# Optimization experiments

Measured on AMD Instinct MI355X. Metric: run time of the kernel, lower is better.

The kernel has to match this reference:

```python
import jax, jax.numpy as jnp
import numpy as np

N_HEAD = 16
D_MODEL = 1024


def setup_inputs() -> dict:
    key = jax.random.key(0)
    ks = jax.random.split(key, 12)
    B, S, D = 2, 2048, D_MODEL
    s = 0.02
    return {
        "q": jax.random.normal(ks[0], (B, S, D), jnp.float32),
        "k": jax.random.normal(ks[1], (B, S, D), jnp.float32),
        "v": jax.random.normal(ks[2], (B, S, 2 * D), jnp.float32),
        "Wq": jax.random.normal(ks[3], (D, D), jnp.float32) * s,
        "bq": jnp.zeros((D,), jnp.float32),
        "Wk": jax.random.normal(ks[4], (D, D), jnp.float32) * s,
        "bk": jnp.zeros((D,), jnp.float32),
        "Wv": jax.random.normal(ks[5], (2 * D, D), jnp.float32) * s,
        "bv": jnp.zeros((D,), jnp.float32),
        "Wfc": jax.random.normal(ks[6], (D, 2 * D), jnp.float32) * s,
        "bfc": jnp.zeros((2 * D,), jnp.float32),
        "padding_mask": jnp.ones((B, S), jnp.int32),
    }


def reference(q, k, v, Wq, bq, Wk, bk, Wv, bv, Wfc, bfc, padding_mask):
    B, S, D = q.shape
    H = N_HEAD
    dh = D // H
    scale = jnp.float32(np.sqrt(dh))
    # projections, split heads -> [B, H, S, dh]
    qh = (q @ Wq + bq).reshape(B, S, H, dh).transpose(0, 2, 1, 3)
    kh = (k @ Wk + bk).reshape(B, S, H, dh).transpose(0, 2, 1, 3)
    vh = (v @ Wv + bv).reshape(B, S, H, dh).transpose(0, 2, 1, 3)
    # scores [B, H, S, S]
    attn = jnp.einsum("bhqd,bhkd->bhqk", qh, kh) / scale
    pad = (padding_mask == 0)[:, None, None, :]  # [B,1,1,S]
    attn = jnp.where(pad, -jnp.inf, attn)
    attn = jax.nn.softmax(attn, axis=-1)
    # dropout p=0 in eval -> identity
    out = jnp.einsum("bhqk,bhkd->bhqd", attn, vh)
    out = out.transpose(0, 2, 1, 3).reshape(B, S, D)
    out = out @ Wfc + bfc  # [B, S, 2D]
    attn_avg = attn.sum(axis=1) / H  # [B, S, S]
    return out, attn_avg
```

## Files before the change

kernel.cpp:

```cpp
#include <hip/hip_runtime.h>
#include <math.h>

#define BATCH   2
#define SLEN    2048
#define DMODEL  1024
#define NHEAD   16
#define DHEAD   64
#define DOUT    2048
#define MROWS   (BATCH * SLEN)
#define NSPLIT  2
#define KSPAN   (SLEN / NSPLIT)

typedef short bf16x8 __attribute__((ext_vector_type(8)));
typedef float floatx4 __attribute__((ext_vector_type(4)));

static __device__ __forceinline__ unsigned short f2bf(float f) {
  unsigned u = __float_as_uint(f);
  u += 0x7fff + ((u >> 16) & 1);
  return (unsigned short)(u >> 16);
}
static __device__ __forceinline__ float bf2f(unsigned short s) {
  return __uint_as_float(((unsigned)s) << 16);
}
static __device__ __forceinline__ floatx4 mfma16(bf16x8 a, bf16x8 b, floatx4 c) {
  return __builtin_amdgcn_mfma_f32_16x16x32_bf16(a, b, c, 0, 0, 0);
}
static __device__ __forceinline__ void gll16(const void* g, void* l) {
  __builtin_amdgcn_global_load_lds(
      (const __attribute__((address_space(1))) unsigned int*)g,
      (__attribute__((address_space(3))) unsigned int*)l, 16, 0, 0);
}

__global__ __launch_bounds__(256) void conv_bf16_k(
    const float* __restrict__ in, unsigned short* __restrict__ out, int n8) {
  const int i = blockIdx.x * 256 + threadIdx.x;
  if (i >= n8) return;
  const float4 a = ((const float4*)in)[i * 2];
  const float4 b = ((const float4*)in)[i * 2 + 1];
  ushort4 u0, u1;
  u0.x = f2bf(a.x); u0.y = f2bf(a.y); u0.z = f2bf(a.z); u0.w = f2bf(a.w);
  u1.x = f2bf(b.x); u1.y = f2bf(b.y); u1.z = f2bf(b.z); u1.w = f2bf(b.w);
  ((ushort4*)out)[i * 2] = u0;
  ((ushort4*)out)[i * 2 + 1] = u1;
}

__global__ __launch_bounds__(256) void wtrans_k(
    const float* __restrict__ W, unsigned short* __restrict__ WT, int K, int N) {
  __shared__ float T[32][33];
  const int t = threadIdx.x;
  const int n0 = blockIdx.x * 32, k0 = blockIdx.y * 32;
  {
    const int r = t >> 3, c4 = (t & 7) * 4;
    const float4 w = *(const float4*)(W + (size_t)(k0 + r) * N + n0 + c4);
    T[r][c4 + 0] = w.x; T[r][c4 + 1] = w.y; T[r][c4 + 2] = w.z; T[r][c4 + 3] = w.w;
  }
  __syncthreads();
  {
    const int n = t >> 3, k4 = (t & 7) * 4;
    ushort4 u;
    u.x = f2bf(T[k4 + 0][n]); u.y = f2bf(T[k4 + 1][n]);
    u.z = f2bf(T[k4 + 2][n]); u.w = f2bf(T[k4 + 3][n]);
    *(ushort4*)(WT + (size_t)(n0 + n) * K + k0 + k4) = u;
  }
}

template <int MODE>
static __device__ __forceinline__ void gemm_body(
    const unsigned short* __restrict__ A, const unsigned short* __restrict__ BT,
    const float* __restrict__ bias, void* __restrict__ C, int M, int K, int N,
    int row0, int col0) {
  __shared__ unsigned short As[128 * 64];
  __shared__ unsigned short Bs[64 * 64];
  const int t = threadIdx.x;
  const int w = t >> 6, l = t & 63, quad = l >> 4, lq = l & 15;
  const int wm = (w >> 1) * 64, wn = (w & 1) * 32;

  const unsigned short* aS[4];
#pragma unroll
  for (int jj = 0; jj < 4; jj++) {
    const int inst = w * 4 + jj;
    const int m = inst * 8 + (l >> 3);
    const int g = l & 7;
    aS[jj] = A + (size_t)(row0 + m) * K + ((g ^ (m & 7)) << 3);
  }
  const unsigned short* bS[2];
#pragma unroll
  for (int jj = 0; jj < 2; jj++) {
    const int inst = w * 2 + jj;
    const int n = inst * 8 + (l >> 3);
    const int g = l & 7;
    bS[jj] = BT + (size_t)(col0 + n) * K + ((g ^ (n & 7)) << 3);
  }

  floatx4 acc[4][2];
#pragma unroll
  for (int i = 0; i < 4; i++)
#pragma unroll
    for (int j = 0; j < 2; j++) acc[i][j] = (floatx4){0.f, 0.f, 0.f, 0.f};

  for (int kt = 0; kt < K; kt += 64) {
#pragma unroll
    for (int jj = 0; jj < 4; jj++)
      gll16(aS[jj] + kt, As + (w * 4 + jj) * 512);
#pragma unroll
    for (int jj = 0; jj < 2; jj++)
      gll16(bS[jj] + kt, Bs + (w * 2 + jj) * 512);
    __syncthreads();

    bf16x8 af[4][2], bfr[2][2];
#pragma unroll
    for (int ti = 0; ti < 4; ti++) {
      const int m = wm + ti * 16 + lq;
#pragma unroll
      for (int h = 0; h < 2; h++)
        af[ti][h] = *(const bf16x8*)(As + m * 64 + (((h * 4 + quad) ^ (m & 7)) << 3));
    }
#pragma unroll
    for (int tj = 0; tj < 2; tj++) {
      const int n = wn + tj * 16 + lq;
#pragma unroll
      for (int h = 0; h < 2; h++)
        bfr[tj][h] = *(const bf16x8*)(Bs + n * 64 + (((h * 4 + quad) ^ (n & 7)) << 3));
    }
#pragma unroll
    for (int ti = 0; ti < 4; ti++)
#pragma unroll
      for (int tj = 0; tj < 2; tj++) {
        acc[ti][tj] = mfma16(af[ti][0], bfr[tj][0], acc[ti][tj]);
        acc[ti][tj] = mfma16(af[ti][1], bfr[tj][1], acc[ti][tj]);
      }
    __syncthreads();
  }

#pragma unroll
  for (int tj = 0; tj < 2; tj++) {
    const int col = col0 + wn + tj * 16 + lq;
    const float bv = bias[col];
    if (MODE == 2) {
#pragma unroll
      for (int ti = 0; ti < 4; ti++) {
        ushort4 u;
        u.x = f2bf(acc[ti][tj][0] + bv);
        u.y = f2bf(acc[ti][tj][1] + bv);
        u.z = f2bf(acc[ti][tj][2] + bv);
        u.w = f2bf(acc[ti][tj][3] + bv);
        *(ushort4*)((unsigned short*)C + (size_t)col * M + row0 + wm + ti * 16 +
                    quad * 4) = u;
      }
    } else {
#pragma unroll
      for (int ti = 0; ti < 4; ti++)
#pragma unroll
        for (int r = 0; r < 4; r++) {
          const int row = row0 + wm + ti * 16 + quad * 4 + r;
          const float vv = acc[ti][tj][r] + bv;
          if (MODE == 1)
            ((float*)C)[(size_t)row * N + col] = vv;
          else
            ((unsigned short*)C)[(size_t)row * N + col] = f2bf(vv);
        }
    }
  }
}

__global__ __launch_bounds__(256) void qkproj_k(
    const unsigned short* qb, const unsigned short* kb,
    const unsigned short* WqT, const unsigned short* WkT,
    const float* bq, const float* bk,
    unsigned short* Qp, unsigned short* Kp) {
  const int z = blockIdx.z;
  gemm_body<0>(z ? kb : qb, z ? WkT : WqT, z ? bk : bq, z ? Kp : Qp,
               MROWS, DMODEL, DMODEL, blockIdx.y * 128, blockIdx.x * 64);
}
__global__ __launch_bounds__(256) void vproj_k(
    const unsigned short* vb, const unsigned short* WvT, const float* bv,
    unsigned short* VT) {
  gemm_body<2>(vb, WvT, bv, VT, MROWS, 2 * DMODEL, DMODEL,
               blockIdx.y * 128, blockIdx.x * 64);
}
__global__ __launch_bounds__(256) void fc_k(
    const unsigned short* att, const unsigned short* WfcT, const float* bfc,
    float* out) {
  gemm_body<1>(att, WfcT, bfc, out, MROWS, DMODEL, DOUT,
               blockIdx.y * 128, blockIdx.x * 64);
}

__global__ __launch_bounds__(256) void flash_mfma_k(
    const unsigned short* __restrict__ Qp, const unsigned short* __restrict__ Kp,
    const unsigned short* __restrict__ VT, const int* __restrict__ mask,
    unsigned short* __restrict__ Opart, float* __restrict__ Lpart) {
  __shared__ unsigned short Ks[64 * 88];
  __shared__ unsigned short Vs[64 * 88];
  __shared__ unsigned short Ps[4 * 16 * 64];
  const int t = threadIdx.x;
  const int w = t >> 6, l = t & 63, quad = l >> 4, lq = l & 15;
  const int q0 = blockIdx.x * 64;
  const int h = blockIdx.y >> 1, split = blockIdx.y & 1;
  const int b = blockIdx.z;

  const unsigned short* qptr =
      Qp + (size_t)(b * SLEN + q0 + w * 16 + lq) * DMODEL + h * 64;
  const bf16x8 aq0 = *(const bf16x8*)(qptr + quad * 8);
  const bf16x8 aq1 = *(const bf16x8*)(qptr + 32 + quad * 8);

  floatx4 acc_o[4];
#pragma unroll
  for (int dj = 0; dj < 4; dj++) acc_o[dj] = (floatx4){0.f, 0.f, 0.f, 0.f};
  float lsum[4] = {0.f, 0.f, 0.f, 0.f};

  const int krow = t >> 2, kseg = (t & 3) * 16;

  for (int k0 = split * KSPAN; k0 < split * KSPAN + KSPAN; k0 += 64) {
    __syncthreads();
    const unsigned short* kg =
        Kp + (size_t)(b * SLEN + k0 + krow) * DMODEL + h * 64 + kseg;
    *(bf16x8*)&Ks[krow * 88 + kseg]     = *(const bf16x8*)kg;
    *(bf16x8*)&Ks[krow * 88 + kseg + 8] = *(const bf16x8*)(kg + 8);
#pragma unroll
    for (int p = 0; p < 2; p++) {
      const int d = (p * 256 + t) >> 3, s8 = (t & 7) * 8;
      *(bf16x8*)&Vs[d * 88 + s8] =
          *(const bf16x8*)(VT + (size_t)(h * 64 + d) * MROWS + b * SLEN + k0 + s8);
    }
    __syncthreads();

    floatx4 s[4];
    int mk[4];
#pragma unroll
    for (int ti = 0; ti < 4; ti++) {
      const bf16x8 bk0 = *(const bf16x8*)&Ks[(ti * 16 + lq) * 88 + quad * 8];
      const bf16x8 bk1 = *(const bf16x8*)&Ks[(ti * 16 + lq) * 88 + 32 + quad * 8];
      floatx4 z = (floatx4){0.f, 0.f, 0.f, 0.f};
      z = mfma16(aq0, bk0, z);
      z = mfma16(aq1, bk1, z);
      s[ti] = z;
      mk[ti] = mask[b * SLEN + k0 + ti * 16 + lq];
    }
#pragma unroll
    for (int ti = 0; ti < 4; ti++)
#pragma unroll
      for (int r = 0; r < 4; r++) {
        float e = __expf(s[ti][r] * 0.125f);
        e = mk[ti] ? e : 0.f;
        s[ti][r] = e;
        lsum[r] += e;
      }
#pragma unroll
    for (int ti = 0; ti < 4; ti++)
#pragma unroll
      for (int r = 0; r < 4; r++) {
        const int qq = quad * 4 + r;
        Ps[w * 1024 + qq * 64 + ((ti * 16 + lq + qq * 8) & 63)] = f2bf(s[ti][r]);
      }
    const bf16x8 ap0 =
        *(const bf16x8*)&Ps[w * 1024 + lq * 64 + 8 * ((quad + lq) & 7)];
    const bf16x8 ap1 =
        *(const bf16x8*)&Ps[w * 1024 + lq * 64 + 8 * ((quad + lq + 4) & 7)];
#pragma unroll
    for (int dj = 0; dj < 4; dj++) {
      const bf16x8 bv0 = *(const bf16x8*)&Vs[(dj * 16 + lq) * 88 + quad * 8];
      const bf16x8 bv1 = *(const bf16x8*)&Vs[(dj * 16 + lq) * 88 + 32 + quad * 8];
      acc_o[dj] = mfma16(ap0, bv0, acc_o[dj]);
      acc_o[dj] = mfma16(ap1, bv1, acc_o[dj]);
    }
  }

#pragma unroll
  for (int r = 0; r < 4; r++) {
    float v = lsum[r];
    v += __shfl_xor(v, 1);
    v += __shfl_xor(v, 2);
    v += __shfl_xor(v, 4);
    v += __shfl_xor(v, 8);
    lsum[r] = v;
  }

  const size_t obase =
      (((size_t)split * BATCH + b) * NHEAD + h) * SLEN + q0 + w * 16;
#pragma unroll
  for (int dj = 0; dj < 4; dj++)
#pragma unroll
    for (int r = 0; r < 4; r++)
      Opart[(obase + quad * 4 + r) * DHEAD + dj * 16 + lq] = f2bf(acc_o[dj][r]);
  if (lq == 0) {
#pragma unroll
    for (int r = 0; r < 4; r++)
      Lpart[obase + quad * 4 + r] = lsum[r];
  }
}

__global__ __launch_bounds__(256) void combine_k(
    const unsigned short* __restrict__ Opart, const float* __restrict__ Lpart,
    unsigned short* __restrict__ att, float* __restrict__ lbuf) {
  const int gid = blockIdx.x * 256 + threadIdx.x;
  const int row = gid >> 3;
  const int d8 = (gid & 7) * 8;
  const float l0 = Lpart[row];
  const float l1 = Lpart[(size_t)BATCH * NHEAD * SLEN + row];
  const float lt = l0 + l1;
  const float il = (lt > 0.f) ? 1.f / lt : 0.f;
  const bf16x8 o0 = *(const bf16x8*)(Opart + (size_t)row * DHEAD + d8);
  const bf16x8 o1 = *(const bf16x8*)(Opart + (size_t)(BATCH * NHEAD * SLEN) * DHEAD +
                                     (size_t)row * DHEAD + d8);
  const int b = row >> 15, hh = (row >> 11) & 15, q = row & 2047;
  unsigned short* dst = att + (size_t)(b * SLEN + q) * DMODEL + hh * 64 + d8;
  ushort4 u0, u1;
  float vv[8];
#pragma unroll
  for (int j = 0; j < 8; j++)
    vv[j] = (bf2f((unsigned short)o0[j]) + bf2f((unsigned short)o1[j])) * il;
  u0.x = f2bf(vv[0]); u0.y = f2bf(vv[1]); u0.z = f2bf(vv[2]); u0.w = f2bf(vv[3]);
  u1.x = f2bf(vv[4]); u1.y = f2bf(vv[5]); u1.z = f2bf(vv[6]); u1.w = f2bf(vv[7]);
  ((ushort4*)dst)[0] = u0;
  ((ushort4*)dst)[1] = u1;
  if ((gid & 7) == 0) lbuf[row] = lt;
}

__global__ __launch_bounds__(256) void attn_avg_mfma_k(
    const unsigned short* __restrict__ Qp, const unsigned short* __restrict__ Kp,
    const float* __restrict__ lbuf, const int* __restrict__ mask,
    float* __restrict__ aout) {
  __shared__ unsigned short Ks[64 * 88];
  const int t = threadIdx.x;
  const int w = t >> 6, l = t & 63, quad = l >> 4, lq = l & 15;
  const int k0 = blockIdx.x * 64, q0 = blockIdx.y * 64, b = blockIdx.z;

  floatx4 acc[4];
#pragma unroll
  for (int ti = 0; ti < 4; ti++) acc[ti] = (floatx4){0.f, 0.f, 0.f, 0.f};
  int mk[4];
#pragma unroll
  for (int ti = 0; ti < 4; ti++) mk[ti] = mask[b * SLEN + k0 + ti * 16 + lq];

  const unsigned short* qbase =
      Qp + (size_t)(b * SLEN + q0 + w * 16 + lq) * DMODEL;
  const int krow = t >> 2, kseg = (t & 3) * 16;

  for (int h = 0; h < NHEAD; h++) {
    __syncthreads();
    const unsigned short* kg =
        Kp + (size_t)(b * SLEN + k0 + krow) * DMODEL + h * 64 + kseg;
    *(bf16x8*)&Ks[krow * 88 + kseg]     = *(const bf16x8*)kg;
    *(bf16x8*)&Ks[krow * 88 + kseg + 8] = *(const bf16x8*)(kg + 8);
    __syncthreads();

    const bf16x8 aq0 = *(const bf16x8*)(qbase + h * 64 + quad * 8);
    const bf16x8 aq1 = *(const bf16x8*)(qbase + h * 64 + 32 + quad * 8);
    float ilr[4];
#pragma unroll
    for (int r = 0; r < 4; r++) {
      const float lv = lbuf[(b * NHEAD + h) * SLEN + q0 + w * 16 + quad * 4 + r];
      ilr[r] = (lv > 0.f) ? 1.f / lv : 0.f;
    }
#pragma unroll
    for (int ti = 0; ti < 4; ti++) {
      const bf16x8 bk0 = *(const bf16x8*)&Ks[(ti * 16 + lq) * 88 + quad * 8];
      const bf16x8 bk1 = *(const bf16x8*)&Ks[(ti * 16 + lq) * 88 + 32 + quad * 8];
      floatx4 z = (floatx4){0.f, 0.f, 0.f, 0.f};
      z = mfma16(aq0, bk0, z);
      z = mfma16(aq1, bk1, z);
#pragma unroll
      for (int r = 0; r < 4; r++)
        acc[ti][r] += mk[ti] ? __expf(z[r] * 0.125f) * ilr[r] : 0.f;
    }
  }
  const float ih = 1.f / NHEAD;
#pragma unroll
  for (int ti = 0; ti < 4; ti++)
#pragma unroll
    for (int r = 0; r < 4; r++)
      aout[(size_t)(b * SLEN + q0 + w * 16 + quad * 4 + r) * SLEN + k0 +
           ti * 16 + lq] = acc[ti][r] * ih;
}

extern "C" void kernel_launch(void* const* d_in, const int* in_sizes, int n_in,
                              void* d_out, int out_size, void* d_ws, size_t ws_size,
                              hipStream_t stream) {
  const float* q   = (const float*)d_in[0];
  const float* k   = (const float*)d_in[1];
  const float* v   = (const float*)d_in[2];
  const float* Wq  = (const float*)d_in[3];
  const float* bq  = (const float*)d_in[4];
  const float* Wk  = (const float*)d_in[5];
  const float* bk  = (const float*)d_in[6];
  const float* Wv  = (const float*)d_in[7];
  const float* bv  = (const float*)d_in[8];
  const float* Wfc = (const float*)d_in[9];
  const float* bfc = (const float*)d_in[10];
  const int* mask  = (const int*)d_in[11];

  float* out      = (float*)d_out;
  float* attn_avg = out + (size_t)MROWS * DOUT;

  unsigned short* qb = (unsigned short*)d_out;
  unsigned short* kb = qb + (1u << 22);
  unsigned short* vb = kb + (1u << 22);
  unsigned short* Opart = (unsigned short*)d_out;
  float* Lpart = (float*)((char*)d_out + (size_t)NSPLIT * BATCH * NHEAD * SLEN * DHEAD * 2);

  unsigned short* wsb  = (unsigned short*)d_ws;
  unsigned short* WqT  = wsb;
  unsigned short* WkT  = wsb + (1u << 20);
  unsigned short* WvT  = wsb + (2u << 20);
  unsigned short* WfcT = wsb + (4u << 20);
  unsigned short* Qp   = wsb + (6u << 20);
  unsigned short* Kp   = Qp + (1u << 22);
  unsigned short* VT   = Kp + (1u << 22);
  unsigned short* att  = VT + (1u << 22);
  float* lbuf = (float*)(att + (1u << 22));

  conv_bf16_k<<<dim3(2048), dim3(256), 0, stream>>>(q, qb, (1 << 22) / 8);
  conv_bf16_k<<<dim3(2048), dim3(256), 0, stream>>>(k, kb, (1 << 22) / 8);
  conv_bf16_k<<<dim3(4096), dim3(256), 0, stream>>>(v, vb, (1 << 23) / 8);
  wtrans_k<<<dim3(32, 32), dim3(256), 0, stream>>>(Wq, WqT, DMODEL, DMODEL);
  wtrans_k<<<dim3(32, 32), dim3(256), 0, stream>>>(Wk, WkT, DMODEL, DMODEL);
  wtrans_k<<<dim3(32, 64), dim3(256), 0, stream>>>(Wv, WvT, 2 * DMODEL, DMODEL);
  wtrans_k<<<dim3(64, 32), dim3(256), 0, stream>>>(Wfc, WfcT, DMODEL, DOUT);
  qkproj_k<<<dim3(DMODEL / 64, MROWS / 128, 2), dim3(256), 0, stream>>>(
      qb, kb, WqT, WkT, bq, bk, Qp, Kp);
  vproj_k<<<dim3(DMODEL / 64, MROWS / 128), dim3(256), 0, stream>>>(
      vb, WvT, bv, VT);
  flash_mfma_k<<<dim3(SLEN / 64, NHEAD * NSPLIT, BATCH), dim3(256), 0, stream>>>(
      Qp, Kp, VT, mask, Opart, Lpart);
  combine_k<<<dim3(BATCH * NHEAD * SLEN * DHEAD / 8 / 256), dim3(256), 0, stream>>>(
      Opart, Lpart, att, lbuf);
  attn_avg_mfma_k<<<dim3(SLEN / 64, SLEN / 64, BATCH), dim3(256), 0, stream>>>(
      Qp, Kp, lbuf, mask, attn_avg);
  fc_k<<<dim3(DOUT / 64, MROWS / 128), dim3(256), 0, stream>>>(
      att, WfcT, bfc, out);
}
```

Baseline: 397.6 us.

## Merge conversion launches and use async swizzled LDS loads in attention kernels

```diff
diff --git a/kernel.cpp b/kernel.cpp
--- a/kernel.cpp
+++ b/kernel.cpp
@@ -31,24 +31,42 @@
       (__attribute__((address_space(3))) unsigned int*)l, 16, 0, 0);
 }
 
-__global__ __launch_bounds__(256) void conv_bf16_k(
-    const float* __restrict__ in, unsigned short* __restrict__ out, int n8) {
-  const int i = blockIdx.x * 256 + threadIdx.x;
-  if (i >= n8) return;
-  const float4 a = ((const float4*)in)[i * 2];
-  const float4 b = ((const float4*)in)[i * 2 + 1];
+__global__ __launch_bounds__(256) void conv_all_k(
+    const float* __restrict__ q, const float* __restrict__ k,
+    const float* __restrict__ v, unsigned short* __restrict__ qb,
+    unsigned short* __restrict__ kb, unsigned short* __restrict__ vb) {
+  int i = blockIdx.x * 256 + threadIdx.x;
+  const float* src;
+  unsigned short* dst;
+  if (i < (1 << 19)) { src = q; dst = qb; }
+  else if (i < (1 << 20)) { src = k; dst = kb; i -= 1 << 19; }
+  else { src = v; dst = vb; i -= 1 << 20; }
+  const float4 a = ((const float4*)src)[i * 2];
+  const float4 b = ((const float4*)src)[i * 2 + 1];
   ushort4 u0, u1;
   u0.x = f2bf(a.x); u0.y = f2bf(a.y); u0.z = f2bf(a.z); u0.w = f2bf(a.w);
   u1.x = f2bf(b.x); u1.y = f2bf(b.y); u1.z = f2bf(b.z); u1.w = f2bf(b.w);
-  ((ushort4*)out)[i * 2] = u0;
-  ((ushort4*)out)[i * 2 + 1] = u1;
-}
-
-__global__ __launch_bounds__(256) void wtrans_k(
-    const float* __restrict__ W, unsigned short* __restrict__ WT, int K, int N) {
+  ((ushort4*)dst)[i * 2] = u0;
+  ((ushort4*)dst)[i * 2 + 1] = u1;
+}
+
+__global__ __launch_bounds__(256) void wtrans_all_k(
+    const float* __restrict__ Wq, const float* __restrict__ Wk,
+    const float* __restrict__ Wv, const float* __restrict__ Wfc,
+    unsigned short* __restrict__ WqT, unsigned short* __restrict__ WkT,
+    unsigned short* __restrict__ WvT, unsigned short* __restrict__ WfcT) {
   __shared__ float T[32][33];
+  int id = blockIdx.x;
+  const float* W;
+  unsigned short* WT;
+  int K, N;
+  if (id < 1024)      { W = Wq;  WT = WqT;  K = 1024; N = 1024; }
+  else if (id < 2048) { W = Wk;  WT = WkT;  K = 1024; N = 1024; id -= 1024; }
+  else if (id < 4096) { W = Wv;  WT = WvT;  K = 2048; N = 1024; id -= 2048; }
+  else                { W = Wfc; WT = WfcT; K = 1024; N = 2048; id -= 4096; }
+  const int ntn = N / 32;
+  const int n0 = (id % ntn) * 32, k0 = (id / ntn) * 32;
   const int t = threadIdx.x;
-  const int n0 = blockIdx.x * 32, k0 = blockIdx.y * 32;
   {
     const int r = t >> 3, c4 = (t & 7) * 4;
     const float4 w = *(const float4*)(W + (size_t)(k0 + r) * N + n0 + c4);
@@ -78,18 +96,14 @@
   const unsigned short* aS[4];
 #pragma unroll
   for (int jj = 0; jj < 4; jj++) {
-    const int inst = w * 4 + jj;
-    const int m = inst * 8 + (l >> 3);
-    const int g = l & 7;
-    aS[jj] = A + (size_t)(row0 + m) * K + ((g ^ (m & 7)) << 3);
+    const int m = (w * 4 + jj) * 8 + (l >> 3);
+    aS[jj] = A + (size_t)(row0 + m) * K + (((l & 7) ^ (m & 7)) << 3);
   }
   const unsigned short* bS[2];
 #pragma unroll
   for (int jj = 0; jj < 2; jj++) {
-    const int inst = w * 2 + jj;
-    const int n = inst * 8 + (l >> 3);
-    const int g = l & 7;
-    bS[jj] = BT + (size_t)(col0 + n) * K + ((g ^ (n & 7)) << 3);
+    const int n = (w * 2 + jj) * 8 + (l >> 3);
+    bS[jj] = BT + (size_t)(col0 + n) * K + (((l & 7) ^ (n & 7)) << 3);
   }
 
   floatx4 acc[4][2];
@@ -189,9 +203,9 @@
     const unsigned short* __restrict__ Qp, const unsigned short* __restrict__ Kp,
     const unsigned short* __restrict__ VT, const int* __restrict__ mask,
     unsigned short* __restrict__ Opart, float* __restrict__ Lpart) {
-  __shared__ unsigned short Ks[64 * 88];
-  __shared__ unsigned short Vs[64 * 88];
-  __shared__ unsigned short Ps[4 * 16 * 64];
+  __shared__ unsigned short Ks[64 * 64];
+  __shared__ unsigned short Vs[64 * 64];
+  __shared__ unsigned short Ps[4][16 * 68];
   const int t = threadIdx.x;
   const int w = t >> 6, l = t & 63, quad = l >> 4, lq = l & 15;
   const int q0 = blockIdx.x * 64;
@@ -203,77 +217,72 @@
   const bf16x8 aq0 = *(const bf16x8*)(qptr + quad * 8);
   const bf16x8 aq1 = *(const bf16x8*)(qptr + 32 + quad * 8);
 
+  int krow[2], kchunk[2];
+#pragma unroll
+  for (int jj = 0; jj < 2; jj++) {
+    krow[jj] = (w * 2 + jj) * 8 + (l >> 3);
+    kchunk[jj] = (l & 7) ^ (krow[jj] & 7);
+  }
+  const unsigned short* Kbase = Kp + (size_t)b * SLEN * DMODEL + h * 64;
+  const unsigned short* Vbase = VT + (size_t)h * 64 * MROWS + b * SLEN;
+
   floatx4 acc_o[4];
 #pragma unroll
   for (int dj = 0; dj < 4; dj++) acc_o[dj] = (floatx4){0.f, 0.f, 0.f, 0.f};
-  float lsum[4] = {0.f, 0.f, 0.f, 0.f};
-
-  const int krow = t >> 2, kseg = (t & 3) * 16;
+  float lsum = 0.f;
+  unsigned short* PsW = &Ps[w][0];
 
   for (int k0 = split * KSPAN; k0 < split * KSPAN + KSPAN; k0 += 64) {
     __syncthreads();
-    const unsigned short* kg =
-        Kp + (size_t)(b * SLEN + k0 + krow) * DMODEL + h * 64 + kseg;
-    *(bf16x8*)&Ks[krow * 88 + kseg]     = *(const bf16x8*)kg;
-    *(bf16x8*)&Ks[krow * 88 + kseg + 8] = *(const bf16x8*)(kg + 8);
-#pragma unroll
-    for (int p = 0; p < 2; p++) {
-      const int d = (p * 256 + t) >> 3, s8 = (t & 7) * 8;
-      *(bf16x8*)&Vs[d * 88 + s8] =
-          *(const bf16x8*)(VT + (size_t)(h * 64 + d) * MROWS + b * SLEN + k0 + s8);
-    }
-    __syncthreads();
-
-    floatx4 s[4];
-    int mk[4];
+#pragma unroll
+    for (int jj = 0; jj < 2; jj++) {
+      const int inst = w * 2 + jj;
+      gll16(Kbase + (size_t)(k0 + krow[jj]) * DMODEL + kchunk[jj] * 8,
+            Ks + inst * 512);
+      gll16(Vbase + (size_t)krow[jj] * MROWS + k0 + kchunk[jj] * 8,
+            Vs + inst * 512);
+    }
+    __syncthreads();
+
 #pragma unroll
     for (int ti = 0; ti < 4; ti++) {
-      const bf16x8 bk0 = *(const bf16x8*)&Ks[(ti * 16 + lq) * 88 + quad * 8];
-      const bf16x8 bk1 = *(const bf16x8*)&Ks[(ti * 16 + lq) * 88 + 32 + quad * 8];
+      const int kk = ti * 16 + lq;
+      const bf16x8 bk0 = *(const bf16x8*)(Ks + kk * 64 + ((quad ^ (kk & 7)) << 3));
+      const bf16x8 bk1 =
+          *(const bf16x8*)(Ks + kk * 64 + (((4 + quad) ^ (kk & 7)) << 3));
       floatx4 z = (floatx4){0.f, 0.f, 0.f, 0.f};
-      z = mfma16(aq0, bk0, z);
-      z = mfma16(aq1, bk1, z);
-      s[ti] = z;
-      mk[ti] = mask[b * SLEN + k0 + ti * 16 + lq];
-    }
-#pragma unroll
-    for (int ti = 0; ti < 4; ti++)
+      z = mfma16(bk0, aq0, z);
+      z = mfma16(bk1, aq1, z);
+      const int4 m4 = *(const int4*)(mask + b * SLEN + k0 + ti * 16 + quad * 4);
+      const int mv[4] = {m4.x, m4.y, m4.z, m4.w};
+      float e[4];
 #pragma unroll
       for (int r = 0; r < 4; r++) {
-        float e = __expf(s[ti][r] * 0.125f);
-        e = mk[ti] ? e : 0.f;
-        s[ti][r] = e;
-        lsum[r] += e;
+        float ev = __expf(z[r] * 0.125f);
+        ev = mv[r] ? ev : 0.f;
+        e[r] = ev;
+        lsum += ev;
       }
-#pragma unroll
-    for (int ti = 0; ti < 4; ti++)
-#pragma unroll
-      for (int r = 0; r < 4; r++) {
-        const int qq = quad * 4 + r;
-        Ps[w * 1024 + qq * 64 + ((ti * 16 + lq + qq * 8) & 63)] = f2bf(s[ti][r]);
-      }
-    const bf16x8 ap0 =
-        *(const bf16x8*)&Ps[w * 1024 + lq * 64 + 8 * ((quad + lq) & 7)];
-    const bf16x8 ap1 =
-        *(const bf16x8*)&Ps[w * 1024 + lq * 64 + 8 * ((quad + lq + 4) & 7)];
+      ushort4 u;
+      u.x = f2bf(e[0]); u.y = f2bf(e[1]); u.z = f2bf(e[2]); u.w = f2bf(e[3]);
+      *(ushort4*)(PsW + lq * 68 + ti * 16 + quad * 4) = u;
+    }
+    __asm__ __volatile__("" ::: "memory");
+    const bf16x8 ap0 = *(const bf16x8*)(PsW + lq * 68 + quad * 8);
+    const bf16x8 ap1 = *(const bf16x8*)(PsW + lq * 68 + 32 + quad * 8);
 #pragma unroll
     for (int dj = 0; dj < 4; dj++) {
-      const bf16x8 bv0 = *(const bf16x8*)&Vs[(dj * 16 + lq) * 88 + quad * 8];
-      const bf16x8 bv1 = *(const bf16x8*)&Vs[(dj * 16 + lq) * 88 + 32 + quad * 8];
+      const int d = dj * 16 + lq;
+      const bf16x8 bv0 = *(const bf16x8*)(Vs + d * 64 + ((quad ^ (d & 7)) << 3));
+      const bf16x8 bv1 =
+          *(const bf16x8*)(Vs + d * 64 + (((4 + quad) ^ (d & 7)) << 3));
       acc_o[dj] = mfma16(ap0, bv0, acc_o[dj]);
       acc_o[dj] = mfma16(ap1, bv1, acc_o[dj]);
     }
   }
 
-#pragma unroll
-  for (int r = 0; r < 4; r++) {
-    float v = lsum[r];
-    v += __shfl_xor(v, 1);
-    v += __shfl_xor(v, 2);
-    v += __shfl_xor(v, 4);
-    v += __shfl_xor(v, 8);
-    lsum[r] = v;
-  }
+  lsum += __shfl_xor(lsum, 16);
+  lsum += __shfl_xor(lsum, 32);
 
   const size_t obase =
       (((size_t)split * BATCH + b) * NHEAD + h) * SLEN + q0 + w * 16;
@@ -282,11 +291,7 @@
 #pragma unroll
     for (int r = 0; r < 4; r++)
       Opart[(obase + quad * 4 + r) * DHEAD + dj * 16 + lq] = f2bf(acc_o[dj][r]);
-  if (lq == 0) {
-#pragma unroll
-    for (int r = 0; r < 4; r++)
-      Lpart[obase + quad * 4 + r] = lsum[r];
-  }
+  if (quad == 0) Lpart[obase + lq] = lsum;
 }
 
 __global__ __launch_bounds__(256) void combine_k(
@@ -320,7 +325,7 @@
     const unsigned short* __restrict__ Qp, const unsigned short* __restrict__ Kp,
     const float* __restrict__ lbuf, const int* __restrict__ mask,
     float* __restrict__ aout) {
-  __shared__ unsigned short Ks[64 * 88];
+  __shared__ unsigned short Ks[64 * 64];
   const int t = threadIdx.x;
   const int w = t >> 6, l = t & 63, quad = l >> 4, lq = l & 15;
   const int k0 = blockIdx.x * 64, q0 = blockIdx.y * 64, b = blockIdx.z;
@@ -332,16 +337,22 @@
 #pragma unroll
   for (int ti = 0; ti < 4; ti++) mk[ti] = mask[b * SLEN + k0 + ti * 16 + lq];
 
+  int krow[2], kchunk[2];
+#pragma unroll
+  for (int jj = 0; jj < 2; jj++) {
+    krow[jj] = (w * 2 + jj) * 8 + (l >> 3);
+    kchunk[jj] = (l & 7) ^ (krow[jj] & 7);
+  }
+  const unsigned short* Kbase = Kp + (size_t)(b * SLEN + k0) * DMODEL;
   const unsigned short* qbase =
       Qp + (size_t)(b * SLEN + q0 + w * 16 + lq) * DMODEL;
-  const int krow = t >> 2, kseg = (t & 3) * 16;
 
   for (int h = 0; h < NHEAD; h++) {
     __syncthreads();
-    const unsigned short* kg =
-        Kp + (size_t)(b * SLEN + k0 + krow) * DMODEL + h * 64 + kseg;
-    *(bf16x8*)&Ks[krow * 88 + kseg]     = *(const bf16x8*)kg;
-    *(bf16x8*)&Ks[krow * 88 + kseg + 8] = *(const bf16x8*)(kg + 8);
+#pragma unroll
+    for (int jj = 0; jj < 2; jj++)
+      gll16(Kbase + (size_t)krow[jj] * DMODEL + h * 64 + kchunk[jj] * 8,
+            Ks + (w * 2 + jj) * 512);
     __syncthreads();
 
     const bf16x8 aq0 = *(const bf16x8*)(qbase + h * 64 + quad * 8);
@@ -354,8 +365,10 @@
     }
 #pragma unroll
     for (int ti = 0; ti < 4; ti++) {
-      const bf16x8 bk0 = *(const bf16x8*)&Ks[(ti * 16 + lq) * 88 + quad * 8];
-      const bf16x8 bk1 = *(const bf16x8*)&Ks[(ti * 16 + lq) * 88 + 32 + quad * 8];
+      const int kk = ti * 16 + lq;
+      const bf16x8 bk0 = *(const bf16x8*)(Ks + kk * 64 + ((quad ^ (kk & 7)) << 3));
+      const bf16x8 bk1 =
+          *(const bf16x8*)(Ks + kk * 64 + (((4 + quad) ^ (kk & 7)) << 3));
       floatx4 z = (floatx4){0.f, 0.f, 0.f, 0.f};
       z = mfma16(aq0, bk0, z);
       z = mfma16(aq1, bk1, z);
@@ -409,13 +422,9 @@
   unsigned short* att  = VT + (1u << 22);
   float* lbuf = (float*)(att + (1u << 22));
 
-  conv_bf16_k<<<dim3(2048), dim3(256), 0, stream>>>(q, qb, (1 << 22) / 8);
-  conv_bf16_k<<<dim3(2048), dim3(256), 0, stream>>>(k, kb, (1 << 22) / 8);
-  conv_bf16_k<<<dim3(4096), dim3(256), 0, stream>>>(v, vb, (1 << 23) / 8);
-  wtrans_k<<<dim3(32, 32), dim3(256), 0, stream>>>(Wq, WqT, DMODEL, DMODEL);
-  wtrans_k<<<dim3(32, 32), dim3(256), 0, stream>>>(Wk, WkT, DMODEL, DMODEL);
-  wtrans_k<<<dim3(32, 64), dim3(256), 0, stream>>>(Wv, WvT, 2 * DMODEL, DMODEL);
-  wtrans_k<<<dim3(64, 32), dim3(256), 0, stream>>>(Wfc, WfcT, DMODEL, DOUT);
+  conv_all_k<<<dim3(8192), dim3(256), 0, stream>>>(q, k, v, qb, kb, vb);
+  wtrans_all_k<<<dim3(6144), dim3(256), 0, stream>>>(Wq, Wk, Wv, Wfc,
+                                                     WqT, WkT, WvT, WfcT);
   qkproj_k<<<dim3(DMODEL / 64, MROWS / 128, 2), dim3(256), 0, stream>>>(
       qb, kb, WqT, WkT, bq, bk, Qp, Kp);
   vproj_k<<<dim3(DMODEL / 64, MROWS / 128), dim3(256), 0, stream>>>(
```

New measurement: 373.3 us. 1.07x faster.
